# Kernel optimization log

Measured on AMD Instinct MI355X. Metric: run time of the kernel, lower is better.

## Reference

```python
import jax, jax.numpy as jnp
import numpy as np

N_CLASS = 4432          # 1108 siRNA classes x 4 cell types
N_GROUPS = 4
GROUP_SIZE = N_CLASS // N_GROUPS  # 1108
LABEL_SMOOTHING = 0.1
CONFIDENCE = 1.0 - LABEL_SMOOTHING
SMOOTHING_VALUE = LABEL_SMOOTHING / (GROUP_SIZE - 1)


def setup_inputs() -> dict:
    key = jax.random.key(0)
    k1, k2 = jax.random.split(key)
    output = jax.random.normal(k1, (16384, N_CLASS), dtype=jnp.float32)
    target = jax.random.randint(k2, (16384,), 0, N_CLASS, dtype=jnp.int64)
    return {"output": output, "target": target}


def reference(output, target):
    # output: [B, C] logits, target: [B] int labels
    log_output = jax.nn.log_softmax(output, axis=1)                      # [B, C]
    classes = jnp.arange(N_CLASS, dtype=target.dtype)                    # [C]
    one_hot = jnp.where(classes[None, :] == target[:, None],
                        CONFIDENCE, SMOOTHING_VALUE).astype(output.dtype)  # [B, C]
    # group of each class (4 cell-type groups, contiguous blocks of GROUP_SIZE)
    class_group = classes // GROUP_SIZE                                  # [C]
    target_group = target // GROUP_SIZE                                  # [B]
    # zero smoothed mass for classes outside the sample's group (masks[group])
    one_hot = jnp.where(class_group[None, :] == target_group[:, None], one_hot, 0.0)
    loss = -(one_hot * log_output).sum(axis=1)                           # [B]
    return jnp.mean(loss)
```

## Files before the change

kernel.cpp:

```cpp
#include <hip/hip_runtime.h>
#include <math.h>

#define N_CLASS   4432
#define GROUP_SZ  1108
#define NV4       (N_CLASS / 4)
#define GV4       (GROUP_SZ / 4)
#define NROWS     16384
#define BLOCK     256
#define FULL_IT   17
#define TAIL_BASE (FULL_IT * 64)
#define TAIL_N    (NV4 - TAIL_BASE)
#define DEPTH     8

static constexpr float CONF   = 0.9f;
static constexpr float SMOOTH = 0.1f / (GROUP_SZ - 1);

typedef float v4f __attribute__((ext_vector_type(4)));

template <bool WS_MODE>
__global__ __launch_bounds__(BLOCK, 8)
void lsl_kernel(const float* __restrict__ logits,
                const int*   __restrict__ target,
                float*       __restrict__ sink) {
    const int wave = threadIdx.x >> 6;
    const int lane = threadIdx.x & 63;
    const int row  = (NROWS - 1) - (blockIdx.x * 4 + wave);
    const v4f* __restrict__ rp = (const v4f*)(logits + (size_t)row * N_CLASS);

    const int t      = __builtin_amdgcn_readfirstlane(target[row]);
    const int g      = t / GROUP_SZ;
    const int glo    = g * GV4;
    const int ghi    = glo + GV4;
    const int tchunk = t >> 2;
    const int tlane  = t & 3;

    v4f buf[DEPTH];
    #pragma unroll
    for (int d = 0; d < DEPTH; ++d)
        buf[d] = __builtin_nontemporal_load(&rp[lane + 64 * d]);

    const bool have18 = (lane < TAIL_N);
    float s = 0.f, gsum = 0.f, xt = 0.f;

    #pragma unroll
    for (int i = 0; i <= FULL_IT; ++i) {
        v4f v = buf[i % DEPTH];
        const int nc = i + DEPTH;
        if (nc < FULL_IT) {
            buf[i % DEPTH] = __builtin_nontemporal_load(&rp[lane + 64 * nc]);
        } else if (nc == FULL_IT) {
            v4f tl = (v4f){-INFINITY, -INFINITY, -INFINITY, -INFINITY};
            if (have18) tl = __builtin_nontemporal_load(&rp[TAIL_BASE + lane]);
            buf[i % DEPTH] = tl;
        }
        const int c = (i < FULL_IT) ? (lane + 64 * i) : (TAIL_BASE + lane);
        s += __expf(v.x) + __expf(v.y) + __expf(v.z) + __expf(v.w);
        if (c >= glo && c < ghi)
            gsum += (v.x + v.y) + (v.z + v.w);
        if (c == tchunk)
            xt = (tlane == 0) ? v.x : (tlane == 1) ? v.y
               : (tlane == 2) ? v.z : v.w;
    }

    #pragma unroll
    for (int off = 32; off > 0; off >>= 1) {
        s    += __shfl_xor(s, off);
        gsum += __shfl_xor(gsum, off);
        xt   += __shfl_xor(xt, off);
    }

    if (lane == 0) {
        const float loss = __logf(s) - ((CONF - SMOOTH) * xt + SMOOTH * gsum);
        if (WS_MODE) sink[row] = loss;
        else         atomicAdd(sink, loss * (1.0f / NROWS));
    }
}

__global__ __launch_bounds__(256)
void lsl_reduce(const float* __restrict__ ws, float* __restrict__ out) {
    const float4* wp = (const float4*)ws;
    const int tid = threadIdx.x;
    float s = 0.f;
    #pragma unroll
    for (int i = 0; i < NROWS / 4 / 256; ++i) {
        float4 v = wp[tid + i * 256];
        s += (v.x + v.y) + (v.z + v.w);
    }
    #pragma unroll
    for (int off = 32; off > 0; off >>= 1) s += __shfl_xor(s, off);
    __shared__ float ss[4];
    const int wave = tid >> 6, lane = tid & 63;
    if (lane == 0) ss[wave] = s;
    __syncthreads();
    if (tid == 0) out[0] = ((ss[0] + ss[1]) + (ss[2] + ss[3])) * (1.0f / NROWS);
}

extern "C" void kernel_launch(void* const* d_in, const int* in_sizes, int n_in,
                              void* d_out, int out_size, void* d_ws, size_t ws_size,
                              hipStream_t stream) {
    const float* logits = (const float*)d_in[0];
    const int*   target = (const int*)d_in[1];
    float*       result = (float*)d_out;
    float*       ws     = (float*)d_ws;

    if (ws_size >= (size_t)NROWS * sizeof(float)) {
        lsl_kernel<true><<<NROWS / 4, BLOCK, 0, stream>>>(logits, target, ws);
        lsl_reduce<<<1, 256, 0, stream>>>(ws, result);
    } else {
        hipMemsetAsync(result, 0, sizeof(float), stream);
        lsl_kernel<false><<<NROWS / 4, BLOCK, 0, stream>>>(logits, target, result);
    }
}
```

Baseline: 386.4 us.

## Process four rows per wave with all row loads issued upfront

Each wave now loops over four consecutive rows instead of handling one, and for each row issues all 18 vector loads before doing any compute. This replaces the depth-8 rolling prefetch buffer. The grid shrinks by four and launch bounds drop to 4 waves per EU so the larger register footprint fits. The aim is more memory-level parallelism per wave and less per-block launch overhead, at the cost of lower occupancy and no overlap of loads between successive rows. The reversed row ordering is also dropped.

```diff
diff --git a/kernel.cpp b/kernel.cpp
--- a/kernel.cpp
+++ b/kernel.cpp
@@ -10,7 +10,7 @@
 #define FULL_IT   17
 #define TAIL_BASE (FULL_IT * 64)
 #define TAIL_N    (NV4 - TAIL_BASE)
-#define DEPTH     8
+#define RPW       4
 
 static constexpr float CONF   = 0.9f;
 static constexpr float SMOOTH = 0.1f / (GROUP_SZ - 1);
@@ -18,61 +18,59 @@
 typedef float v4f __attribute__((ext_vector_type(4)));
 
 template <bool WS_MODE>
-__global__ __launch_bounds__(BLOCK, 8)
+__global__ __launch_bounds__(BLOCK, 4)
 void lsl_kernel(const float* __restrict__ logits,
                 const int*   __restrict__ target,
                 float*       __restrict__ sink) {
     const int wave = threadIdx.x >> 6;
     const int lane = threadIdx.x & 63;
-    const int row  = (NROWS - 1) - (blockIdx.x * 4 + wave);
-    const v4f* __restrict__ rp = (const v4f*)(logits + (size_t)row * N_CLASS);
+    const int wid  = blockIdx.x * 4 + wave;
+    const int base = wid * RPW;
+    const bool have18 = (lane < TAIL_N);
 
-    const int t      = __builtin_amdgcn_readfirstlane(target[row]);
-    const int g      = t / GROUP_SZ;
-    const int glo    = g * GV4;
-    const int ghi    = glo + GV4;
-    const int tchunk = t >> 2;
-    const int tlane  = t & 3;
+    #pragma unroll 1
+    for (int r = 0; r < RPW; ++r) {
+        const int row = base + r;
+        const v4f* __restrict__ rp = (const v4f*)(logits + (size_t)row * N_CLASS);
 
-    v4f buf[DEPTH];
-    #pragma unroll
-    for (int d = 0; d < DEPTH; ++d)
-        buf[d] = __builtin_nontemporal_load(&rp[lane + 64 * d]);
+        v4f v[FULL_IT + 1];
+        #pragma unroll
+        for (int i = 0; i < FULL_IT; ++i)
+            v[i] = __builtin_nontemporal_load(&rp[lane + 64 * i]);
+        v[FULL_IT] = (v4f){-INFINITY, -INFINITY, -INFINITY, -INFINITY};
+        if (have18) v[FULL_IT] = __builtin_nontemporal_load(&rp[TAIL_BASE + lane]);
 
-    const bool have18 = (lane < TAIL_N);
-    float s = 0.f, gsum = 0.f, xt = 0.f;
+        const int t      = target[row];
+        const int g      = t / GROUP_SZ;
+        const int glo    = g * GV4;
+        const int tchunk = t >> 2;
+        const int tlane  = t & 3;
 
-    #pragma unroll
-    for (int i = 0; i <= FULL_IT; ++i) {
-        v4f v = buf[i % DEPTH];
-        const int nc = i + DEPTH;
-        if (nc < FULL_IT) {
-            buf[i % DEPTH] = __builtin_nontemporal_load(&rp[lane + 64 * nc]);
-        } else if (nc == FULL_IT) {
-            v4f tl = (v4f){-INFINITY, -INFINITY, -INFINITY, -INFINITY};
-            if (have18) tl = __builtin_nontemporal_load(&rp[TAIL_BASE + lane]);
-            buf[i % DEPTH] = tl;
+        float s = 0.f, gsum = 0.f, xt = 0.f;
+        #pragma unroll
+        for (int i = 0; i <= FULL_IT; ++i) {
+            const v4f x = v[i];
+            s += __expf(x.x) + __expf(x.y) + __expf(x.z) + __expf(x.w);
+            const int c = (i < FULL_IT) ? (lane + 64 * i) : (TAIL_BASE + lane);
+            if ((unsigned)(c - glo) < (unsigned)GV4)
+                gsum += (x.x + x.y) + (x.z + x.w);
+            if (c == tchunk)
+                xt = (tlane == 0) ? x.x : (tlane == 1) ? x.y
+                   : (tlane == 2) ? x.z : x.w;
         }
-        const int c = (i < FULL_IT) ? (lane + 64 * i) : (TAIL_BASE + lane);
-        s += __expf(v.x) + __expf(v.y) + __expf(v.z) + __expf(v.w);
-        if (c >= glo && c < ghi)
-            gsum += (v.x + v.y) + (v.z + v.w);
-        if (c == tchunk)
-            xt = (tlane == 0) ? v.x : (tlane == 1) ? v.y
-               : (tlane == 2) ? v.z : v.w;
-    }
 
-    #pragma unroll
-    for (int off = 32; off > 0; off >>= 1) {
-        s    += __shfl_xor(s, off);
-        gsum += __shfl_xor(gsum, off);
-        xt   += __shfl_xor(xt, off);
-    }
+        #pragma unroll
+        for (int off = 32; off > 0; off >>= 1) {
+            s    += __shfl_xor(s, off);
+            gsum += __shfl_xor(gsum, off);
+            xt   += __shfl_xor(xt, off);
+        }
 
-    if (lane == 0) {
-        const float loss = __logf(s) - ((CONF - SMOOTH) * xt + SMOOTH * gsum);
-        if (WS_MODE) sink[row] = loss;
-        else         atomicAdd(sink, loss * (1.0f / NROWS));
+        if (lane == 0) {
+            const float loss = __logf(s) - ((CONF - SMOOTH) * xt + SMOOTH * gsum);
+            if (WS_MODE) sink[row] = loss;
+            else         atomicAdd(sink, loss * (1.0f / NROWS));
+        }
     }
 }
 
@@ -104,10 +102,10 @@
     float*       ws     = (float*)d_ws;
 
     if (ws_size >= (size_t)NROWS * sizeof(float)) {
-        lsl_kernel<true><<<NROWS / 4, BLOCK, 0, stream>>>(logits, target, ws);
+        lsl_kernel<true><<<NROWS / (4 * RPW), BLOCK, 0, stream>>>(logits, target, ws);
         lsl_reduce<<<1, 256, 0, stream>>>(ws, result);
     } else {
         hipMemsetAsync(result, 0, sizeof(float), stream);
-        lsl_kernel<false><<<NROWS / 4, BLOCK, 0, stream>>>(logits, target, result);
+        lsl_kernel<false><<<NROWS / (4 * RPW), BLOCK, 0, stream>>>(logits, target, result);
     }
 }
```

After: 359.3 us. 1.08x faster.
